# Performance work log

Measured on AMD Instinct MI355X. Metric: run time of the kernel, lower is better.

The kernel has to match this reference:

```python
import jax, jax.numpy as jnp
import numpy as np

N0, N1, E, B = 100000, 100000, 800000, 1024
F0, F1 = 93, 43


def _gin(x, src, dst, w, b, n):
    # GINConv(eps=0): h_i = Lin(x_i + sum_{j->i} x_j)
    agg = jax.ops.segment_sum(x[src], dst, num_segments=n)
    return (x + agg) @ w + b


def _pool(x, batch, num_graphs):
    s = jax.ops.segment_sum(x, batch, num_segments=num_graphs)
    cnt = jax.ops.segment_sum(jnp.ones((x.shape[0],), x.dtype), batch, num_segments=num_graphs)
    mean = s / jnp.maximum(cnt, 1.0)[:, None]
    mx = jax.ops.segment_max(x, batch, num_segments=num_graphs)
    return jnp.concatenate([mean, mx], axis=1)


def _pairnorm(x, eps=1e-5):
    x = x - x.mean(axis=0, keepdims=True)
    return x / jnp.sqrt(eps + (x * x).sum(-1).mean())


def _bn(x, gamma, beta, eps=1e-5):
    mu = x.mean(axis=0, keepdims=True)
    var = x.var(axis=0, keepdims=True)
    return (x - mu) / jnp.sqrt(var + eps) * gamma + beta


def _branch(x, ei, batch, n, wc_a, bc_a, wc_b, bc_b, fg_w1, fg_b1, fg_w2, fg_b2, fg_g, fg_bt, ff_w1, ff_b1, ff_w2, ff_b2):
    src, dst = ei[0], ei[1]
    h = jax.nn.relu(_gin(x, src, dst, wc_a, bc_a, n))
    h = jax.nn.relu(_gin(h, src, dst, wc_b, bc_b, n))
    g = _pairnorm(_pool(h, batch, B))
    g = jax.nn.relu(g @ fg_w1 + fg_b1)
    g = _bn(g @ fg_w2 + fg_b2, fg_g, fg_bt)  # [B, 512]
    z = jax.nn.relu(g @ ff_w1 + ff_b1)
    z = jax.nn.sigmoid(z @ ff_w2 + ff_b2)  # [B, 2]
    return z[:, 0], z[:, 1], g


def setup_inputs() -> dict:
    key = jax.random.key(0)
    ks = iter(jax.random.split(key, 40))

    def lin(fan_in, fan_out):
        bnd = 1.0 / np.sqrt(fan_in)
        w = jax.random.uniform(next(ks), (fan_in, fan_out), jnp.float32, -bnd, bnd)
        b = jax.random.uniform(next(ks), (fan_out,), jnp.float32, -bnd, bnd)
        return w, b

    x0 = jax.random.normal(next(ks), (N0, F0), jnp.float32)
    x1 = jax.random.normal(next(ks), (N1, F1), jnp.float32)
    ei0 = jax.random.randint(next(ks), (2, E), 0, N0, jnp.int32)
    ei1 = jax.random.randint(next(ks), (2, E), 0, N1, jnp.int32)
    b0 = jnp.sort(jax.random.randint(next(ks), (N0,), 0, B, jnp.int32))
    b1 = jnp.sort(jax.random.randint(next(ks), (N1,), 0, B, jnp.int32))

    inp = {"x0": x0, "edge_index_0": ei0, "batch_0": b0, "x1": x1, "edge_index_1": ei1, "batch_1": b1}
    inp["w_c1"], inp["b_c1"] = lin(F0, F0)
    inp["w_c2"], inp["b_c2"] = lin(F0, F0 * 10)
    inp["w_c3"], inp["b_c3"] = lin(F1, F1)
    inp["w_c4"], inp["b_c4"] = lin(F1, F1 * 10)
    inp["fg0_w1"], inp["fg0_b1"] = lin(F0 * 10 * 2, 1024)
    inp["fg0_w2"], inp["fg0_b2"] = lin(1024, 512)
    inp["fg0_g"], inp["fg0_bt"] = jnp.ones((512,), jnp.float32), jnp.zeros((512,), jnp.float32)
    inp["fg1_w1"], inp["fg1_b1"] = lin(F1 * 10 * 2, 1024)
    inp["fg1_w2"], inp["fg1_b2"] = lin(1024, 512)
    inp["fg1_g"], inp["fg1_bt"] = jnp.ones((512,), jnp.float32), jnp.zeros((512,), jnp.float32)
    inp["ff0_w1"], inp["ff0_b1"] = lin(512, 256)
    inp["ff0_w2"], inp["ff0_b2"] = lin(256, 2)
    inp["ff1_w1"], inp["ff1_b1"] = lin(512, 256)
    inp["ff1_w2"], inp["ff1_b2"] = lin(256, 2)
    return inp


def reference(x0, edge_index_0, batch_0, x1, edge_index_1, batch_1,
              w_c1, b_c1, w_c2, b_c2, w_c3, b_c3, w_c4, b_c4,
              fg0_w1, fg0_b1, fg0_w2, fg0_b2, fg0_g, fg0_bt,
              fg1_w1, fg1_b1, fg1_w2, fg1_b2, fg1_g, fg1_bt,
              ff0_w1, ff0_b1, ff0_w2, ff0_b2,
              ff1_w1, ff1_b1, ff1_w2, ff1_b2):
    alpha, beta, xg0 = _branch(x0, edge_index_0, batch_0, N0, w_c1, b_c1, w_c2, b_c2,
                               fg0_w1, fg0_b1, fg0_w2, fg0_b2, fg0_g, fg0_bt,
                               ff0_w1, ff0_b1, ff0_w2, ff0_b2)
    alpha1, beta1, xg1 = _branch(x1, edge_index_1, batch_1, N1, w_c3, b_c3, w_c4, b_c4,
                                 fg1_w1, fg1_b1, fg1_w2, fg1_b2, fg1_g, fg1_bt,
                                 ff1_w1, ff1_b1, ff1_w2, ff1_b2)
    return (alpha, beta, xg0, xg1, alpha1, beta1)
```

## Files before the change

### kernel.cpp

```cpp
#include <hip/hip_runtime.h>
#include <hip/hip_bf16.h>
#include <math.h>

#define EDGES 800000
#define NNODES 100000
#define NGRAPH 1024
#define SCAN_B 256

typedef __attribute__((ext_vector_type(8))) short short8v;
typedef __attribute__((ext_vector_type(4))) float float4v;
typedef unsigned short ushort_t;

__device__ inline ushort_t f2bf(float f) {
  __hip_bfloat16 h = __float2bfloat16(f);
  return *reinterpret_cast<ushort_t*>(&h);
}
__device__ inline float bf2f(ushort_t u) {
  return __uint_as_float(((unsigned int)u) << 16);
}

__global__ __launch_bounds__(256) void deg_k(const int* __restrict__ dst,
                                             int* __restrict__ deg, int E) {
  int e = blockIdx.x * 256 + threadIdx.x;
  if (e < E) atomicAdd(&deg[dst[e]], 1);
}

__global__ __launch_bounds__(SCAN_B) void scan_block_k(const int* __restrict__ deg,
                                                       int* __restrict__ scanned,
                                                       int* __restrict__ bsum, int n) {
  __shared__ int tmp[SCAN_B];
  int b = blockIdx.x, t = threadIdx.x, i = b * SCAN_B + t;
  int v = (i < n) ? deg[i] : 0;
  tmp[t] = v;
  __syncthreads();
  for (int off = 1; off < SCAN_B; off <<= 1) {
    int x = (t >= off) ? tmp[t - off] : 0;
    __syncthreads();
    tmp[t] += x;
    __syncthreads();
  }
  if (i < n) scanned[i] = tmp[t] - v;
  if (t == SCAN_B - 1) bsum[b] = tmp[t];
}

__global__ __launch_bounds__(512) void scan_sums_k(int* __restrict__ bsum, int nb) {
  __shared__ int tmp[512];
  int t = threadIdx.x;
  int v = (t < nb) ? bsum[t] : 0;
  tmp[t] = v;
  __syncthreads();
  for (int off = 1; off < 512; off <<= 1) {
    int x = (t >= off) ? tmp[t - off] : 0;
    __syncthreads();
    tmp[t] += x;
    __syncthreads();
  }
  if (t < nb) bsum[t] = tmp[t] - v;
}

__global__ __launch_bounds__(256) void scan_add_k(const int* __restrict__ scanned,
                                                  const int* __restrict__ bsum,
                                                  int* __restrict__ rowstart, int n,
                                                  int total) {
  int i = blockIdx.x * 256 + threadIdx.x;
  if (i < n) rowstart[i] = scanned[i] + bsum[i / SCAN_B];
  if (i == 0) rowstart[n] = total;
}

__global__ __launch_bounds__(256) void fill_k(const int* __restrict__ src,
                                              const int* __restrict__ dst,
                                              const int* __restrict__ rowstart,
                                              int* __restrict__ cur,
                                              int* __restrict__ adj, int E) {
  int e = blockIdx.x * 256 + threadIdx.x;
  if (e >= E) return;
  int d = dst[e];
  int p = rowstart[d] + atomicAdd(&cur[d], 1);
  adj[p] = src[e];
}

__global__ __launch_bounds__(256) void gstart_k(const int* __restrict__ bat,
                                                int* __restrict__ gs, int N, int B) {
  int g = blockIdx.x * 256 + threadIdx.x;
  if (g > B) return;
  if (g == B) {
    gs[B] = N;
    return;
  }
  int lo = 0, hi = N;
  while (lo < hi) {
    int mid = (lo + hi) >> 1;
    if (bat[mid] < g) lo = mid + 1;
    else hi = mid;
  }
  gs[g] = lo;
}

template <int KP>
__global__ __launch_bounds__(256) void tobf16_k(const float* __restrict__ x,
                                                ushort_t* __restrict__ out, int M,
                                                int F) {
  long i = (long)blockIdx.x * 256 + threadIdx.x;
  if (i >= (long)M * KP) return;
  int r = (int)(i / KP), c = (int)(i % KP);
  float v = (c < F) ? x[(long)r * F + c] : 0.f;
  out[i] = f2bf(v);
}

template <int KP>
__global__ __launch_bounds__(256) void gather_k(const ushort_t* __restrict__ X,
                                                const int* __restrict__ rowstart,
                                                const int* __restrict__ adj,
                                                ushort_t* __restrict__ out, int M) {
  constexpr int CH = KP / 8;
  long tid = (long)blockIdx.x * 256 + threadIdx.x;
  if (tid >= (long)M * CH) return;
  int node = (int)(tid / CH), ch = (int)(tid % CH);
  int o = ch * 8;
  float acc[8];
  uint4 self = *(const uint4*)&X[(long)node * KP + o];
  {
    const unsigned int u[4] = {self.x, self.y, self.z, self.w};
#pragma unroll
    for (int i = 0; i < 4; ++i) {
      acc[2 * i] = __uint_as_float((u[i] & 0xFFFFu) << 16);
      acc[2 * i + 1] = __uint_as_float(u[i] & 0xFFFF0000u);
    }
  }
  int rs = rowstart[node], re = rowstart[node + 1];
  for (int e = rs; e < re; ++e) {
    int j = adj[e];
    uint4 v = *(const uint4*)&X[(long)j * KP + o];
    const unsigned int u[4] = {v.x, v.y, v.z, v.w};
#pragma unroll
    for (int i = 0; i < 4; ++i) {
      acc[2 * i] += __uint_as_float((u[i] & 0xFFFFu) << 16);
      acc[2 * i + 1] += __uint_as_float(u[i] & 0xFFFF0000u);
    }
  }
  uint4 r;
  unsigned int* p = &r.x;
#pragma unroll
  for (int i = 0; i < 4; ++i) {
    unsigned int lo = f2bf(acc[2 * i]);
    unsigned int hi = f2bf(acc[2 * i + 1]);
    p[i] = lo | (hi << 16);
  }
  *(uint4*)&out[(long)node * KP + o] = r;
}

__global__ __launch_bounds__(256) void wt_k(const float* __restrict__ W,
                                            ushort_t* __restrict__ WT, int K, int N,
                                            int KP, int Npad) {
  int i = blockIdx.x * 256 + threadIdx.x;
  if (i >= Npad * KP) return;
  int n = i / KP, k = i % KP;
  float v = (k < K && n < N) ? W[(long)k * N + n] : 0.f;
  WT[i] = f2bf(v);
}

template <int KP>
__global__ __launch_bounds__(256) void conv_gemm2_k(
    const ushort_t* __restrict__ A, const ushort_t* __restrict__ WT,
    const float* __restrict__ bias, ushort_t* __restrict__ Cout, int M, int Nc,
    int OW, int NT) {
  constexpr int NKS = KP / 32;
  int tid = threadIdx.x;
  int wid = tid >> 6, lane = tid & 63;
  int lr = lane & 15, q = lane >> 4;
  int lk = q * 8;
  int row0 = blockIdx.x * 64;
  int arow = row0 + wid * 16 + lr;

  short8v a[NKS];
  const ushort_t* ap = A + (long)arow * KP + lk;
#pragma unroll
  for (int ks = 0; ks < NKS; ++ks) a[ks] = *(const short8v*)(ap + ks * 32);

  for (int ct = 0; ct < NT; ++ct) {
    int col0 = ct * 64;
    float4v acc[4];
#pragma unroll
    for (int i = 0; i < 4; ++i) acc[i] = (float4v){0.f, 0.f, 0.f, 0.f};
#pragma unroll
    for (int ks = 0; ks < NKS; ++ks) {
#pragma unroll
      for (int nf = 0; nf < 4; ++nf) {
        short8v b =
            *(const short8v*)&WT[(long)(col0 + nf * 16 + lr) * KP + ks * 32 + lk];
        acc[nf] = __builtin_amdgcn_mfma_f32_16x16x32_bf16(a[ks], b, acc[nf], 0, 0, 0);
      }
    }
#pragma unroll
    for (int nf = 0; nf < 4; ++nf) {
      int gc = col0 + nf * 16 + lr;
      if (gc >= OW) continue;
      float bv = (gc < Nc) ? bias[gc] : 0.f;
#pragma unroll
      for (int i = 0; i < 4; ++i) {
        int gr = row0 + wid * 16 + q * 4 + i;
        if (gr < M) {
          float v = (gc < Nc) ? fmaxf(acc[nf][i] + bv, 0.f) : 0.f;
          Cout[(long)gr * OW + gc] = f2bf(v);
        }
      }
    }
  }
}

template <int KP, int NT>
__global__ __launch_bounds__(256) void conv_pool_k(
    const ushort_t* __restrict__ A, const ushort_t* __restrict__ WT,
    const float* __restrict__ bias, const int* __restrict__ gstart,
    float* __restrict__ pool, int Nc, int NCpool) {
  constexpr int NKS = KP / 32;
  constexpr int MAXR = 192;
  constexpr int CH = KP / 8;
  constexpr int LDW = KP + 8;
  constexpr int MAXT = (NT + 3) / 4;
  __shared__ ushort_t Asl[MAXR * LDW];

  int g = blockIdx.x;
  int rs = gstart[g], re = gstart[g + 1];
  int rows = re - rs;
  int tid = threadIdx.x;
  int wid = tid >> 6, lane = tid & 63;
  int lr = lane & 15, q = lane >> 4, lk = q * 8;

  float ssum[MAXT][4];
  float smax[MAXT][4];
#pragma unroll
  for (int t = 0; t < MAXT; ++t)
#pragma unroll
    for (int nf = 0; nf < 4; ++nf) {
      ssum[t][nf] = 0.f;
      smax[t][nf] = 0.f;
    }

  int nwin = (rows + MAXR - 1) / MAXR;
  for (int w = 0; w < nwin; ++w) {
    int base = rs + w * MAXR;
    int wr = min(MAXR, re - base);
    for (int i = tid; i < wr * CH; i += 256) {
      int r = i / CH, cc = i % CH;
      *(uint4*)&Asl[r * LDW + cc * 8] = *(const uint4*)&A[(long)(base + r) * KP + cc * 8];
    }
    __syncthreads();
    int nch = (wr + 15) / 16;
#pragma unroll
    for (int t = 0; t < MAXT; ++t) {
      int ct = wid + t * 4;
      if (ct < NT) {
        int col0 = ct * 64;
        short8v bfr[NKS][4];
        float bv[4];
#pragma unroll
        for (int nf = 0; nf < 4; ++nf) {
          int gc = col0 + nf * 16 + lr;
          bv[nf] = (gc < Nc) ? bias[gc] : 0.f;
#pragma unroll
          for (int ks = 0; ks < NKS; ++ks)
            bfr[ks][nf] =
                *(const short8v*)&WT[(long)(col0 + nf * 16 + lr) * KP + ks * 32 + lk];
        }
        for (int c = 0; c < nch; ++c) {
          float4v acc[4];
#pragma unroll
          for (int i = 0; i < 4; ++i) acc[i] = (float4v){0.f, 0.f, 0.f, 0.f};
#pragma unroll
          for (int ks = 0; ks < NKS; ++ks) {
            short8v a = *(const short8v*)&Asl[(c * 16 + lr) * LDW + ks * 32 + lk];
#pragma unroll
            for (int nf = 0; nf < 4; ++nf)
              acc[nf] = __builtin_amdgcn_mfma_f32_16x16x32_bf16(a, bfr[ks][nf],
                                                                acc[nf], 0, 0, 0);
          }
          int rbase = c * 16 + q * 4;
#pragma unroll
          for (int nf = 0; nf < 4; ++nf) {
            float v0 = (rbase + 0 < wr) ? fmaxf(acc[nf][0] + bv[nf], 0.f) : 0.f;
            float v1 = (rbase + 1 < wr) ? fmaxf(acc[nf][1] + bv[nf], 0.f) : 0.f;
            float v2 = (rbase + 2 < wr) ? fmaxf(acc[nf][2] + bv[nf], 0.f) : 0.f;
            float v3 = (rbase + 3 < wr) ? fmaxf(acc[nf][3] + bv[nf], 0.f) : 0.f;
            float s = (v0 + v1) + (v2 + v3);
            float m = fmaxf(fmaxf(v0, v1), fmaxf(v2, v3));
            s += __shfl_xor(s, 16);
            s += __shfl_xor(s, 32);
            m = fmaxf(m, __shfl_xor(m, 16));
            m = fmaxf(m, __shfl_xor(m, 32));
            ssum[t][nf] += s;
            smax[t][nf] = fmaxf(smax[t][nf], m);
          }
        }
      }
    }
    __syncthreads();
  }

  float inv = 1.f / fmaxf((float)rows, 1.f);
  if (q == 0) {
#pragma unroll
    for (int t = 0; t < MAXT; ++t) {
      int ct = wid + t * 4;
      if (ct < NT) {
#pragma unroll
        for (int nf = 0; nf < 4; ++nf) {
          int gc = ct * 64 + nf * 16 + lr;
          if (gc < Nc) {
            pool[(long)g * 2 * NCpool + gc] = ssum[t][nf] * inv;
            pool[(long)g * 2 * NCpool + NCpool + gc] = smax[t][nf];
          }
        }
      }
    }
  }
}

__global__ __launch_bounds__(256) void fc_mfma_k(const ushort_t* __restrict__ A,
                                                 const ushort_t* __restrict__ WT,
                                                 float* __restrict__ PART, int KP,
                                                 int Nc, int Kc) {
  int tid = threadIdx.x;
  int wid = tid >> 6, lane = tid & 63;
  int lr = lane & 15, q = lane >> 4, lk = q * 8;
  int row0 = blockIdx.y * 64, col0 = blockIdx.x * 64;
  int M = gridDim.y * 64;
  int kbeg = blockIdx.z * Kc;
  int arow = row0 + wid * 16 + lr;
  const ushort_t* ap = A + (long)arow * KP + kbeg + lk;
  const ushort_t* wp = WT + (long)col0 * KP + kbeg + lk;

  float4v acc[4];
#pragma unroll
  for (int i = 0; i < 4; ++i) acc[i] = (float4v){0.f, 0.f, 0.f, 0.f};

  for (int k0 = 0; k0 < Kc; k0 += 32) {
    short8v a = *(const short8v*)(ap + k0);
#pragma unroll
    for (int nf = 0; nf < 4; ++nf) {
      short8v b = *(const short8v*)(wp + (long)(nf * 16 + lr) * KP + k0);
      acc[nf] = __builtin_amdgcn_mfma_f32_16x16x32_bf16(a, b, acc[nf], 0, 0, 0);
    }
  }

  float* P = PART + (long)blockIdx.z * M * Nc;
#pragma unroll
  for (int nf = 0; nf < 4; ++nf) {
    int gc = col0 + nf * 16 + lr;
#pragma unroll
    for (int i = 0; i < 4; ++i) {
      int gr = row0 + wid * 16 + q * 4 + i;
      P[(long)gr * Nc + gc] = acc[nf][i];
    }
  }
}

__global__ __launch_bounds__(256) void sk_epi2_k(const float* __restrict__ PART,
                                                 const float* __restrict__ bias,
                                                 float* __restrict__ Cf,
                                                 ushort_t* __restrict__ Cb, int M,
                                                 int Nc, int SK, int relu) {
  long idx = (long)blockIdx.x * 256 + threadIdx.x;
  if (idx >= (long)M * Nc) return;
  int c = (int)(idx % Nc);
  float s = bias[c];
  for (int z = 0; z < SK; ++z) s += PART[(long)z * M * Nc + idx];
  if (relu) s = fmaxf(s, 0.f);
  if (Cf) Cf[idx] = s;
  if (Cb) Cb[idx] = f2bf(s);
}

__global__ __launch_bounds__(256) void colstat_part_k(const float* __restrict__ X,
                                                      float* __restrict__ PS,
                                                      float* __restrict__ ssqtot,
                                                      int Rows, int Cols, int CR) {
  __shared__ float sred[256];
  int c0 = blockIdx.x * 64;
  int chunk = blockIdx.y;
  int t = threadIdx.x;
  int c = c0 + (t & 63);
  int rg = t >> 6;
  int rbeg = chunk * CR, rend = min(Rows, rbeg + CR);
  float s = 0.f, s2 = 0.f;
  if (c < Cols) {
    for (int r = rbeg + rg; r < rend; r += 4) {
      float v = X[(long)r * Cols + c];
      s += v;
      s2 += v * v;
    }
  }
  sred[t] = s;
  __syncthreads();
  if (t < 64 && c0 + t < Cols)
    PS[(long)chunk * Cols + c0 + t] = sred[t] + sred[t + 64] + sred[t + 128] + sred[t + 192];
  for (int off = 32; off > 0; off >>= 1) s2 += __shfl_down(s2, off);
  if ((t & 63) == 0) atomicAdd(ssqtot, s2);
}

__global__ __launch_bounds__(256) void colstat_fin_k(const float* __restrict__ PS,
                                                     float* __restrict__ cm, int Rows,
                                                     int Cols, int nchunk) {
  int c = blockIdx.x * 256 + threadIdx.x;
  if (c >= Cols) return;
  float s = 0.f;
  for (int z = 0; z < nchunk; ++z) s += PS[(long)z * Cols + c];
  cm[c] = s / Rows;
}

__global__ __launch_bounds__(256) void pn_scale_k(const float* __restrict__ cm,
                                                  const float* __restrict__ ssqtot,
                                                  float* __restrict__ scale, int Rows,
                                                  int Cols) {
  __shared__ float red[256];
  int t = threadIdx.x;
  float s = 0.f;
  for (int i = t; i < Cols; i += 256) {
    float v = cm[i];
    s += v * v;
  }
  red[t] = s;
  __syncthreads();
  for (int off = 128; off > 0; off >>= 1) {
    if (t < off) red[t] += red[t + off];
    __syncthreads();
  }
  if (t == 0) {
    float ssq = ssqtot[0] - (float)Rows * red[0];
    scale[0] = 1.f / sqrtf(1e-5f + ssq / Rows);
  }
}

__global__ __launch_bounds__(256) void pn_apply2_k(const float* __restrict__ X,
                                                   const float* __restrict__ cm,
                                                   const float* __restrict__ scale,
                                                   ushort_t* __restrict__ outB,
                                                   int Rows, int Cols, int KP1) {
  long idx = (long)blockIdx.x * 256 + threadIdx.x;
  if (idx >= (long)Rows * KP1) return;
  int r = (int)(idx / KP1), c = (int)(idx % KP1);
  float v = 0.f;
  if (c < Cols) v = (X[(long)r * Cols + c] - cm[c]) * scale[0];
  outB[idx] = f2bf(v);
}

__global__ __launch_bounds__(256) void bn_part_k(const float* __restrict__ X,
                                                 float* __restrict__ PS,
                                                 float* __restrict__ PQ, int Rows,
                                                 int Cols, int CR) {
  __shared__ float s1[256], s2l[256];
  int c0 = blockIdx.x * 64;
  int chunk = blockIdx.y;
  int t = threadIdx.x;
  int c = c0 + (t & 63);
  int rg = t >> 6;
  int rbeg = chunk * CR, rend = min(Rows, rbeg + CR);
  float a = 0.f, b = 0.f;
  if (c < Cols) {
    for (int r = rbeg + rg; r < rend; r += 4) {
      float v = X[(long)r * Cols + c];
      a += v;
      b += v * v;
    }
  }
  s1[t] = a;
  s2l[t] = b;
  __syncthreads();
  if (t < 64 && c0 + t < Cols) {
    PS[(long)chunk * Cols + c0 + t] = s1[t] + s1[t + 64] + s1[t + 128] + s1[t + 192];
    PQ[(long)chunk * Cols + c0 + t] = s2l[t] + s2l[t + 64] + s2l[t + 128] + s2l[t + 192];
  }
}

__global__ __launch_bounds__(256) void bn_fin_k(const float* __restrict__ PS,
                                                const float* __restrict__ PQ,
                                                float* __restrict__ mu,
                                                float* __restrict__ var, int Rows,
                                                int Cols, int nchunk) {
  int c = blockIdx.x * 256 + threadIdx.x;
  if (c >= Cols) return;
  float s = 0.f, q = 0.f;
  for (int z = 0; z < nchunk; ++z) {
    s += PS[(long)z * Cols + c];
    q += PQ[(long)z * Cols + c];
  }
  float m = s / Rows;
  mu[c] = m;
  var[c] = q / Rows - m * m;
}

__global__ void bn_apply2_k(float* __restrict__ X, const float* __restrict__ mu,
                            const float* __restrict__ var, const float* __restrict__ g,
                            const float* __restrict__ b, ushort_t* __restrict__ XB16,
                            int Rows, int Cols) {
  long idx = (long)blockIdx.x * 256 + threadIdx.x;
  if (idx >= (long)Rows * Cols) return;
  int c = (int)(idx % Cols);
  float v = (X[idx] - mu[c]) / sqrtf(var[c] + 1e-5f) * g[c] + b[c];
  X[idx] = v;
  XB16[idx] = f2bf(v);
}

__global__ __launch_bounds__(64) void ff2_k(const ushort_t* __restrict__ Z,
                                            const float* __restrict__ W2,
                                            const float* __restrict__ b2,
                                            float* __restrict__ alpha,
                                            float* __restrict__ beta, int K) {
  int row = blockIdx.x;
  int t = threadIdx.x;
  float s0 = 0.f, s1 = 0.f;
  for (int k = t; k < K; k += 64) {
    float z = bf2f(Z[(long)row * K + k]);
    s0 += z * W2[2 * k];
    s1 += z * W2[2 * k + 1];
  }
  for (int off = 32; off > 0; off >>= 1) {
    s0 += __shfl_down(s0, off);
    s1 += __shfl_down(s1, off);
  }
  if (t == 0) {
    alpha[row] = 1.f / (1.f + expf(-(s0 + b2[0])));
    beta[row] = 1.f / (1.f + expf(-(s1 + b2[1])));
  }
}

template <int KP, int NTT>
static void run_branch(const float* x, const int* ei, const int* bat,
                       const float* wc1, const float* bc1, const float* wc2,
                       const float* bc2, const float* fgw1, const float* fgb1,
                       const float* fgw2, const float* fgb2, const float* fgg,
                       const float* fgbt, const float* ffw1, const float* ffb1,
                       const float* ffw2, const float* ffb2, int N, int F,
                       float* out_alpha, float* out_beta, float* out_xg,
                       ushort_t* XB, ushort_t* XA, ushort_t* H, ushort_t* WT,
                       int* deg, int* scanned, int* rowstart, int* cur, int* bsum,
                       int* adj, int* GS, float* POOL, float* CM, float* MU,
                       float* VAR, float* SSQ, float* PSUM, float* PSQ,
                       ushort_t* POOLB, ushort_t* WTF1, ushort_t* WTF2,
                       ushort_t* WTFF, ushort_t* G1B, ushort_t* XGB, ushort_t* Z1B,
                       float* PART, hipStream_t stream) {
  const int NC = F * 10;
  const int Bn = NGRAPH;
  const int* src = ei;
  const int* dst = ei + EDGES;
  const int MB = (N + 63) / 64;
  const int Mpad = MB * 64;
  const int nb = (N + SCAN_B - 1) / SCAN_B;

  hipMemsetAsync(deg, 0, (size_t)N * 4, stream);
  hipMemsetAsync(cur, 0, (size_t)N * 4, stream);
  deg_k<<<(EDGES + 255) / 256, 256, 0, stream>>>(dst, deg, EDGES);
  scan_block_k<<<nb, SCAN_B, 0, stream>>>(deg, scanned, bsum, N);
  scan_sums_k<<<1, 512, 0, stream>>>(bsum, nb);
  scan_add_k<<<nb, 256, 0, stream>>>(scanned, bsum, rowstart, N, EDGES);
  fill_k<<<(EDGES + 255) / 256, 256, 0, stream>>>(src, dst, rowstart, cur, adj, EDGES);
  gstart_k<<<(NGRAPH + 256) / 256, 256, 0, stream>>>(bat, GS, N, NGRAPH);

  constexpr int CH = KP / 8;
  if (Mpad > N)
    hipMemsetAsync(XA + (size_t)N * KP, 0, (size_t)(Mpad - N) * KP * 2, stream);
  tobf16_k<KP><<<(int)(((long)N * KP + 255) / 256), 256, 0, stream>>>(x, XB, N, F);
  gather_k<KP><<<(int)(((long)N * CH + 255) / 256), 256, 0, stream>>>(XB, rowstart, adj, XA, N);
  wt_k<<<(((F + 63) / 64) * 64 * KP + 255) / 256, 256, 0, stream>>>(
      wc1, WT, F, F, KP, ((F + 63) / 64) * 64);
  conv_gemm2_k<KP><<<MB, 256, 0, stream>>>(XA, WT, bc1, H, N, F, KP, (KP + 63) / 64);
  gather_k<KP><<<(int)(((long)N * CH + 255) / 256), 256, 0, stream>>>(H, rowstart, adj, XA, N);
  int Npad2 = ((NC + 63) / 64) * 64;
  wt_k<<<(Npad2 * KP + 255) / 256, 256, 0, stream>>>(wc2, WT, F, NC, KP, Npad2);
  conv_pool_k<KP, NTT><<<NGRAPH, 256, 0, stream>>>(XA, WT, bc2, GS, POOL, NC, NC);

  int Cols = 2 * NC;
  const int NCH = 16, CR = NGRAPH / NCH;
  hipMemsetAsync(SSQ, 0, 8, stream);
  colstat_part_k<<<dim3((Cols + 63) / 64, NCH), 256, 0, stream>>>(POOL, PSUM, SSQ, Bn, Cols, CR);
  colstat_fin_k<<<(Cols + 255) / 256, 256, 0, stream>>>(PSUM, CM, Bn, Cols, NCH);
  pn_scale_k<<<1, 256, 0, stream>>>(CM, SSQ, SSQ + 1, Bn, Cols);

  int KP1 = ((Cols + 127) / 128) * 128;
  pn_apply2_k<<<(int)(((long)Bn * KP1 + 255) / 256), 256, 0, stream>>>(
      POOL, CM, SSQ + 1, POOLB, Bn, Cols, KP1);
  wt_k<<<(1024 * KP1 + 255) / 256, 256, 0, stream>>>(fgw1, WTF1, Cols, 1024, KP1, 1024);
  fc_mfma_k<<<dim3(16, 16, 4), 256, 0, stream>>>(POOLB, WTF1, PART, KP1, 1024, KP1 / 4);
  sk_epi2_k<<<(Bn * 1024 + 255) / 256, 256, 0, stream>>>(PART, fgb1, nullptr, G1B, Bn, 1024, 4, 1);
  wt_k<<<(512 * 1024 + 255) / 256, 256, 0, stream>>>(fgw2, WTF2, 1024, 512, 1024, 512);
  fc_mfma_k<<<dim3(8, 16, 4), 256, 0, stream>>>(G1B, WTF2, PART, 1024, 512, 256);
  sk_epi2_k<<<(Bn * 512 + 255) / 256, 256, 0, stream>>>(PART, fgb2, out_xg, nullptr, Bn, 512, 4, 0);
  bn_part_k<<<dim3(8, 8), 256, 0, stream>>>(out_xg, PSUM, PSQ, Bn, 512, 128);
  bn_fin_k<<<2, 256, 0, stream>>>(PSUM, PSQ, MU, VAR, Bn, 512, 8);
  bn_apply2_k<<<(Bn * 512 + 255) / 256, 256, 0, stream>>>(out_xg, MU, VAR, fgg, fgbt, XGB, Bn, 512);
  wt_k<<<(256 * 512 + 255) / 256, 256, 0, stream>>>(ffw1, WTFF, 512, 256, 512, 256);
  fc_mfma_k<<<dim3(4, 16, 8), 256, 0, stream>>>(XGB, WTFF, PART, 512, 256, 64);
  sk_epi2_k<<<(Bn * 256 + 255) / 256, 256, 0, stream>>>(PART, ffb1, nullptr, Z1B, Bn, 256, 8, 1);
  ff2_k<<<Bn, 64, 0, stream>>>(Z1B, ffw2, ffb2, out_alpha, out_beta, 256);
}

extern "C" void kernel_launch(void* const* d_in, const int* in_sizes, int n_in,
                              void* d_out, int out_size, void* d_ws, size_t ws_size,
                              hipStream_t stream) {
  if (n_in < 34) return;
  const float* x0 = (const float*)d_in[0];
  const int* ei0 = (const int*)d_in[1];
  const int* b0 = (const int*)d_in[2];
  const float* x1 = (const float*)d_in[3];
  const int* ei1 = (const int*)d_in[4];
  const int* b1 = (const int*)d_in[5];
  const float* w_c1 = (const float*)d_in[6];
  const float* b_c1 = (const float*)d_in[7];
  const float* w_c2 = (const float*)d_in[8];
  const float* b_c2 = (const float*)d_in[9];
  const float* w_c3 = (const float*)d_in[10];
  const float* b_c3 = (const float*)d_in[11];
  const float* w_c4 = (const float*)d_in[12];
  const float* b_c4 = (const float*)d_in[13];
  const float* fg0_w1 = (const float*)d_in[14];
  const float* fg0_b1 = (const float*)d_in[15];
  const float* fg0_w2 = (const float*)d_in[16];
  const float* fg0_b2 = (const float*)d_in[17];
  const float* fg0_g = (const float*)d_in[18];
  const float* fg0_bt = (const float*)d_in[19];
  const float* fg1_w1 = (const float*)d_in[20];
  const float* fg1_b1 = (const float*)d_in[21];
  const float* fg1_w2 = (const float*)d_in[22];
  const float* fg1_b2 = (const float*)d_in[23];
  const float* fg1_g = (const float*)d_in[24];
  const float* fg1_bt = (const float*)d_in[25];
  const float* ff0_w1 = (const float*)d_in[26];
  const float* ff0_b1 = (const float*)d_in[27];
  const float* ff0_w2 = (const float*)d_in[28];
  const float* ff0_b2 = (const float*)d_in[29];
  const float* ff1_w1 = (const float*)d_in[30];
  const float* ff1_b1 = (const float*)d_in[31];
  const float* ff1_w2 = (const float*)d_in[32];
  const float* ff1_b2 = (const float*)d_in[33];

  float* out = (float*)d_out;
  float* alpha = out;
  float* beta = out + 1024;
  float* xg0 = out + 2048;
  float* xg1 = out + 2048 + 1024 * 512;
  float* alpha1 = out + 2048 + 2 * 1024 * 512;
  float* beta1 = alpha1 + 1024;

  char* w = (char*)d_ws;
  auto alloc = [&](size_t bytes) -> void* {
    void* p = (void*)w;
    w += ((bytes + 255) / 256) * 256;
    return p;
  };
  const int Mpad = ((NNODES + 63) / 64) * 64;
  ushort_t* XB = (ushort_t*)alloc((size_t)Mpad * 96 * 2);
  ushort_t* XA = (ushort_t*)alloc((size_t)Mpad * 96 * 2);
  ushort_t* H = (ushort_t*)alloc((size_t)Mpad * 96 * 2);
  ushort_t* WT = (ushort_t*)alloc((size_t)960 * 96 * 2);
  int* deg = (int*)alloc((size_t)(NNODES + 1) * 4);
  int* scanned = (int*)alloc((size_t)(NNODES + 1) * 4);
  int* rowstart = (int*)alloc((size_t)(NNODES + 1) * 4);
  int* cur = (int*)alloc((size_t)NNODES * 4);
  int* bsum = (int*)alloc(512 * 4);
  int* adj = (int*)alloc((size_t)EDGES * 4);
  int* GS = (int*)alloc((size_t)(NGRAPH + 1) * 4);
  float* POOL = (float*)alloc((size_t)NGRAPH * 1860 * 4);
  float* CM = (float*)alloc(1860 * 4);
  float* MU = (float*)alloc(512 * 4);
  float* VAR = (float*)alloc(512 * 4);
  float* SSQ = (float*)alloc(256);
  float* PSUM = (float*)alloc((size_t)16 * 1920 * 4);
  float* PSQ = (float*)alloc((size_t)8 * 512 * 4);
  ushort_t* POOLB = (ushort_t*)alloc((size_t)NGRAPH * 1920 * 2);
  ushort_t* WTF1 = (ushort_t*)alloc((size_t)1024 * 1920 * 2);
  ushort_t* WTF2 = (ushort_t*)alloc((size_t)512 * 1024 * 2);
  ushort_t* WTFF = (ushort_t*)alloc((size_t)256 * 512 * 2);
  ushort_t* G1B = (ushort_t*)alloc((size_t)NGRAPH * 1024 * 2);
  ushort_t* XGB = (ushort_t*)alloc((size_t)NGRAPH * 512 * 2);
  ushort_t* Z1B = (ushort_t*)alloc((size_t)NGRAPH * 256 * 2);
  if ((size_t)(w - (char*)d_ws) > ws_size) return;

  float* PART = (float*)XB;

  run_branch<96, 15>(x0, ei0, b0, w_c1, b_c1, w_c2, b_c2, fg0_w1, fg0_b1, fg0_w2,
                     fg0_b2, fg0_g, fg0_bt, ff0_w1, ff0_b1, ff0_w2, ff0_b2, NNODES,
                     93, alpha, beta, xg0, XB, XA, H, WT, deg, scanned, rowstart,
                     cur, bsum, adj, GS, POOL, CM, MU, VAR, SSQ, PSUM, PSQ, POOLB,
                     WTF1, WTF2, WTFF, G1B, XGB, Z1B, PART, stream);
  run_branch<64, 7>(x1, ei1, b1, w_c3, b_c3, w_c4, b_c4, fg1_w1, fg1_b1, fg1_w2,
                    fg1_b2, fg1_g, fg1_bt, ff1_w1, ff1_b1, ff1_w2, ff1_b2, NNODES,
                    43, alpha1, beta1, xg1, XB, XA, H, WT, deg, scanned, rowstart,
                    cur, bsum, adj, GS, POOL, CM, MU, VAR, SSQ, PSUM, PSQ, POOLB,
                    WTF1, WTF2, WTFF, G1B, XGB, Z1B, PART, stream);
}
```

Baseline: 725.1 us.

## Bucket edges by destination block before CSR fill; defer pool shuffles per window

The CSR fill becomes two passes. First each block buckets its edges by destination block of 256 nodes, using shared-memory histograms and a global bucket cursor, and writes (src,dst) pairs into a staging buffer aliased onto XB. Then a fill pass does the per-node atomics and adj writes with much better locality than random scatter. The conv_pool kernel now accumulates per-lane partial sums and maxes across row chunks and does the cross-lane shuffles once per window instead of per chunk. It also shrinks the shared row window from 192 to 128 and skips the final barrier. The cost is an extra kernel and extra edge traffic, plus more windows for large graphs.

```diff
diff --git a/kernel.cpp b/kernel.cpp
--- a/kernel.cpp
+++ b/kernel.cpp
@@ -67,16 +67,45 @@
   if (i == 0) rowstart[n] = total;
 }
 
-__global__ __launch_bounds__(256) void fill_k(const int* __restrict__ src,
-                                              const int* __restrict__ dst,
-                                              const int* __restrict__ rowstart,
-                                              int* __restrict__ cur,
-                                              int* __restrict__ adj, int E) {
+#define NBMAX 512
+__global__ __launch_bounds__(256) void bscatter_k(const int* __restrict__ src,
+                                                  const int* __restrict__ dst,
+                                                  const int* __restrict__ rowstart,
+                                                  int* __restrict__ bcur,
+                                                  int2* __restrict__ EB, int E,
+                                                  int NB) {
+  __shared__ int hist[NBMAX], run[NBMAX], lcur[NBMAX];
+  int t = threadIdx.x;
+  for (int b = t; b < NB; b += 256) {
+    hist[b] = 0;
+    lcur[b] = 0;
+  }
+  __syncthreads();
+  int e0 = blockIdx.x * 4096;
+  int e1 = min(E, e0 + 4096);
+  for (int e = e0 + t; e < e1; e += 256) atomicAdd(&hist[dst[e] >> 8], 1);
+  __syncthreads();
+  for (int b = t; b < NB; b += 256)
+    if (hist[b] > 0) run[b] = atomicAdd(&bcur[b], hist[b]);
+  __syncthreads();
+  for (int e = e0 + t; e < e1; e += 256) {
+    int d = dst[e];
+    int b = d >> 8;
+    int l = atomicAdd(&lcur[b], 1);
+    int pos = rowstart[b << 8] + run[b] + l;
+    EB[pos] = make_int2(src[e], d);
+  }
+}
+
+__global__ __launch_bounds__(256) void fill2_k(const int2* __restrict__ EB,
+                                               const int* __restrict__ rowstart,
+                                               int* __restrict__ cur,
+                                               int* __restrict__ adj, int E) {
   int e = blockIdx.x * 256 + threadIdx.x;
   if (e >= E) return;
-  int d = dst[e];
-  int p = rowstart[d] + atomicAdd(&cur[d], 1);
-  adj[p] = src[e];
+  int2 ed = EB[e];
+  int p = rowstart[ed.y] + atomicAdd(&cur[ed.y], 1);
+  adj[p] = ed.x;
 }
 
 __global__ __launch_bounds__(256) void gstart_k(const int* __restrict__ bat,
@@ -214,7 +243,7 @@
     const float* __restrict__ bias, const int* __restrict__ gstart,
     float* __restrict__ pool, int Nc, int NCpool) {
   constexpr int NKS = KP / 32;
-  constexpr int MAXR = 192;
+  constexpr int MAXR = 128;
   constexpr int CH = KP / 8;
   constexpr int LDW = KP + 8;
   constexpr int MAXT = (NT + 3) / 4;
@@ -263,6 +292,14 @@
             bfr[ks][nf] =
                 *(const short8v*)&WT[(long)(col0 + nf * 16 + lr) * KP + ks * 32 + lk];
         }
+        float wsum[4][4], wmax[4][4];
+#pragma unroll
+        for (int nf = 0; nf < 4; ++nf)
+#pragma unroll
+          for (int i = 0; i < 4; ++i) {
+            wsum[nf][i] = 0.f;
+            wmax[nf][i] = 0.f;
+          }
         for (int c = 0; c < nch; ++c) {
           float4v acc[4];
 #pragma unroll
@@ -277,24 +314,29 @@
           }
           int rbase = c * 16 + q * 4;
 #pragma unroll
-          for (int nf = 0; nf < 4; ++nf) {
-            float v0 = (rbase + 0 < wr) ? fmaxf(acc[nf][0] + bv[nf], 0.f) : 0.f;
-            float v1 = (rbase + 1 < wr) ? fmaxf(acc[nf][1] + bv[nf], 0.f) : 0.f;
-            float v2 = (rbase + 2 < wr) ? fmaxf(acc[nf][2] + bv[nf], 0.f) : 0.f;
-            float v3 = (rbase + 3 < wr) ? fmaxf(acc[nf][3] + bv[nf], 0.f) : 0.f;
-            float s = (v0 + v1) + (v2 + v3);
-            float m = fmaxf(fmaxf(v0, v1), fmaxf(v2, v3));
-            s += __shfl_xor(s, 16);
-            s += __shfl_xor(s, 32);
-            m = fmaxf(m, __shfl_xor(m, 16));
-            m = fmaxf(m, __shfl_xor(m, 32));
-            ssum[t][nf] += s;
-            smax[t][nf] = fmaxf(smax[t][nf], m);
-          }
+          for (int nf = 0; nf < 4; ++nf)
+#pragma unroll
+            for (int i = 0; i < 4; ++i) {
+              float v = (rbase + i < wr) ? fmaxf(acc[nf][i] + bv[nf], 0.f) : 0.f;
+              wsum[nf][i] += v;
+              wmax[nf][i] = fmaxf(wmax[nf][i], v);
+            }
+        }
+#pragma unroll
+        for (int nf = 0; nf < 4; ++nf) {
+          float s = (wsum[nf][0] + wsum[nf][1]) + (wsum[nf][2] + wsum[nf][3]);
+          float m = fmaxf(fmaxf(wmax[nf][0], wmax[nf][1]),
+                          fmaxf(wmax[nf][2], wmax[nf][3]));
+          s += __shfl_xor(s, 16);
+          s += __shfl_xor(s, 32);
+          m = fmaxf(m, __shfl_xor(m, 16));
+          m = fmaxf(m, __shfl_xor(m, 32));
+          ssum[t][nf] += s;
+          smax[t][nf] = fmaxf(smax[t][nf], m);
         }
       }
     }
-    __syncthreads();
+    if (w + 1 < nwin) __syncthreads();
   }
 
   float inv = 1.f / fmaxf((float)rows, 1.f);
@@ -533,8 +575,8 @@
                        float* out_alpha, float* out_beta, float* out_xg,
                        ushort_t* XB, ushort_t* XA, ushort_t* H, ushort_t* WT,
                        int* deg, int* scanned, int* rowstart, int* cur, int* bsum,
-                       int* adj, int* GS, float* POOL, float* CM, float* MU,
-                       float* VAR, float* SSQ, float* PSUM, float* PSQ,
+                       int* bcur, int* adj, int* GS, float* POOL, float* CM,
+                       float* MU, float* VAR, float* SSQ, float* PSUM, float* PSQ,
                        ushort_t* POOLB, ushort_t* WTF1, ushort_t* WTF2,
                        ushort_t* WTFF, ushort_t* G1B, ushort_t* XGB, ushort_t* Z1B,
                        float* PART, hipStream_t stream) {
@@ -545,14 +587,18 @@
   const int MB = (N + 63) / 64;
   const int Mpad = MB * 64;
   const int nb = (N + SCAN_B - 1) / SCAN_B;
-
+  const int NB = (N + 255) >> 8;
+
+  int2* EB = (int2*)XB;
   hipMemsetAsync(deg, 0, (size_t)N * 4, stream);
   hipMemsetAsync(cur, 0, (size_t)N * 4, stream);
+  hipMemsetAsync(bcur, 0, NBMAX * 4, stream);
   deg_k<<<(EDGES + 255) / 256, 256, 0, stream>>>(dst, deg, EDGES);
   scan_block_k<<<nb, SCAN_B, 0, stream>>>(deg, scanned, bsum, N);
   scan_sums_k<<<1, 512, 0, stream>>>(bsum, nb);
   scan_add_k<<<nb, 256, 0, stream>>>(scanned, bsum, rowstart, N, EDGES);
-  fill_k<<<(EDGES + 255) / 256, 256, 0, stream>>>(src, dst, rowstart, cur, adj, EDGES);
+  bscatter_k<<<(EDGES + 4095) / 4096, 256, 0, stream>>>(src, dst, rowstart, bcur, EB, EDGES, NB);
+  fill2_k<<<(EDGES + 255) / 256, 256, 0, stream>>>(EB, rowstart, cur, adj, EDGES);
   gstart_k<<<(NGRAPH + 256) / 256, 256, 0, stream>>>(bat, GS, N, NGRAPH);
 
   constexpr int CH = KP / 8;
@@ -656,6 +702,7 @@
   int* rowstart = (int*)alloc((size_t)(NNODES + 1) * 4);
   int* cur = (int*)alloc((size_t)NNODES * 4);
   int* bsum = (int*)alloc(512 * 4);
+  int* bcur = (int*)alloc(NBMAX * 4);
   int* adj = (int*)alloc((size_t)EDGES * 4);
   int* GS = (int*)alloc((size_t)(NGRAPH + 1) * 4);
   float* POOL = (float*)alloc((size_t)NGRAPH * 1860 * 4);
@@ -679,11 +726,11 @@
   run_branch<96, 15>(x0, ei0, b0, w_c1, b_c1, w_c2, b_c2, fg0_w1, fg0_b1, fg0_w2,
                      fg0_b2, fg0_g, fg0_bt, ff0_w1, ff0_b1, ff0_w2, ff0_b2, NNODES,
                      93, alpha, beta, xg0, XB, XA, H, WT, deg, scanned, rowstart,
-                     cur, bsum, adj, GS, POOL, CM, MU, VAR, SSQ, PSUM, PSQ, POOLB,
-                     WTF1, WTF2, WTFF, G1B, XGB, Z1B, PART, stream);
+                     cur, bsum, bcur, adj, GS, POOL, CM, MU, VAR, SSQ, PSUM, PSQ,
+                     POOLB, WTF1, WTF2, WTFF, G1B, XGB, Z1B, PART, stream);
   run_branch<64, 7>(x1, ei1, b1, w_c3, b_c3, w_c4, b_c4, fg1_w1, fg1_b1, fg1_w2,
                     fg1_b2, fg1_g, fg1_bt, ff1_w1, ff1_b1, ff1_w2, ff1_b2, NNODES,
                     43, alpha1, beta1, xg1, XB, XA, H, WT, deg, scanned, rowstart,
-                    cur, bsum, adj, GS, POOL, CM, MU, VAR, SSQ, PSUM, PSQ, POOLB,
-                    WTF1, WTF2, WTFF, G1B, XGB, Z1B, PART, stream);
-}
+                    cur, bsum, bcur, adj, GS, POOL, CM, MU, VAR, SSQ, PSUM, PSQ,
+                    POOLB, WTF1, WTF2, WTFF, G1B, XGB, Z1B, PART, stream);
+}
```

Result: no change. 721.2 us (-0.5%).
